# Kernel tuning notes

Hardware: AMD Instinct MI355X
Metric: run time of the kernel (lower is better)

The kernel has to match this reference:

```python
import jax, jax.numpy as jnp
import numpy as np

WS = 16      # window_size
FW = 1       # focal_window -> 3x3 grid of focal windows
FF = 2       # focal_factor (avg-pool for non-center windows)
NH = 8       # num_heads

_OFFSETS = [(di, dj) for di in range(-FW, FW + 1) for dj in range(-FW, FW + 1)]
# tokens contributed by each focal window (center keeps full res, neighbors pooled)
_COUNTS = np.array([WS * WS if (di == 0 and dj == 0) else (WS // FF) ** 2 for di, dj in _OFFSETS])
# center window gets zero bias, peripheral windows get -position_bias (intent of add_focal_bias)
_MULTS = np.array([0.0 if (di == 0 and dj == 0) else -1.0 for di, dj in _OFFSETS], dtype=np.float32)


def _gather_focal(x):
    """x: (B,H,W,C) -> (B*nW, kv_len, C) focal key/value tokens per window."""
    B, H, W, C = x.shape
    nH, nWg = H // WS, W // WS
    xp = jnp.pad(x, ((0, 0), (WS, WS), (WS, WS), (0, 0)), mode='reflect')
    # padded window grid: (B, nH+2, nWg+2, WS, WS, C)
    g = xp.reshape(B, nH + 2, WS, nWg + 2, WS, C).transpose(0, 1, 3, 2, 4, 5)
    parts = []
    for di, dj in _OFFSETS:
        w = g[:, 1 + di:1 + di + nH, 1 + dj:1 + dj + nWg]  # (B,nH,nWg,WS,WS,C)
        if di == 0 and dj == 0:
            t = w.reshape(B, nH, nWg, WS * WS, C)
        else:
            p = WS // FF  # avg_pool2d(kernel=stride=FF)
            t = w.reshape(B, nH, nWg, p, FF, p, FF, C).mean(axis=(4, 6)).reshape(B, nH, nWg, p * p, C)
        parts.append(t)
    kv = jnp.concatenate(parts, axis=3)  # (B,nH,nWg,kv_len,C)
    return kv.reshape(B * nH * nWg, -1, C)


def _bias_tokens(position_bias):
    # (NH, 9) -> (NH, kv_len): per-focal-window bias broadcast over its tokens
    scaled = position_bias * jnp.asarray(_MULTS)[None, :]
    return jnp.repeat(scaled, _COUNTS, axis=1)


def reference(x, Wq, bq, Wk, bk, Wv, bv, Wo, bo, position_bias):
    B, H, W, C = x.shape
    hd = C // NH
    scale = hd ** -0.5
    nH, nWg = H // WS, W // WS
    # window partition: (B*nW, WS*WS, C)
    xw = x.reshape(B, nH, WS, nWg, WS, C).transpose(0, 1, 3, 2, 4, 5).reshape(-1, WS * WS, C)
    kv = _gather_focal(x)  # (B*nW, kv_len, C)
    q = (xw @ Wq + bq).reshape(-1, WS * WS, NH, hd).transpose(0, 2, 1, 3)
    k = (kv @ Wk + bk).reshape(kv.shape[0], -1, NH, hd).transpose(0, 2, 1, 3)
    v = (kv @ Wv + bv).reshape(kv.shape[0], -1, NH, hd).transpose(0, 2, 1, 3)
    attn = jnp.einsum('whqd,whkd->whqk', q, k) * scale
    attn = attn + _bias_tokens(position_bias)[None, :, None, :]
    attn = jax.nn.softmax(attn, axis=-1)
    out = jnp.einsum('whqk,whkd->whqd', attn, v).transpose(0, 2, 1, 3).reshape(-1, WS * WS, C)
    out = out @ Wo + bo
    # window reverse
    out = out.reshape(B, nH, nWg, WS, WS, C).transpose(0, 1, 3, 2, 4, 5).reshape(B, H, W, C)
    return out


def setup_inputs() -> dict:
    key = jax.random.key(0)
    ks = jax.random.split(key, 10)
    D = 384
    w = lambda k: jax.random.normal(k, (D, D), dtype=jnp.float32) * 0.02
    b = lambda k: jax.random.normal(k, (D,), dtype=jnp.float32) * 0.02
    return {
        'x': jax.random.normal(ks[0], (2, 128, 128, D), dtype=jnp.float32),
        'Wq': w(ks[1]), 'bq': b(ks[2]),
        'Wk': w(ks[3]), 'bk': b(ks[4]),
        'Wv': w(ks[5]), 'bv': b(ks[6]),
        'Wo': w(ks[7]), 'bo': b(ks[8]),
        'position_bias': jax.random.normal(ks[9], (NH, 9), dtype=jnp.float32) * 0.02,
    }
```

## Files before the change

### kernel.cpp

```cpp
#include <hip/hip_runtime.h>
#include <hip/hip_bf16.h>

#define NTOK 32768
#define LOG2E 1.4426950408889634f

typedef __attribute__((ext_vector_type(8))) short bf16x8;
typedef __attribute__((ext_vector_type(4))) float f32x4;

__device__ __forceinline__ float bf2f(unsigned short u) {
  return __uint_as_float(((unsigned int)u) << 16);
}
__device__ __forceinline__ unsigned short f2bf(float f) {
  union { __hip_bfloat16 h; unsigned short u; } cv;
  cv.h = __float2bfloat16(f);
  return cv.u;
}
__device__ __forceinline__ unsigned cvt_pk_bf16(float lo, float hi) {
  unsigned r;
  asm("v_cvt_pk_bf16_f32 %0, %1, %2" : "=v"(r) : "v"(lo), "v"(hi));
  return r;
}
__device__ __forceinline__ float fast_exp2(float x) {
#if __has_builtin(__builtin_amdgcn_exp2f)
  return __builtin_amdgcn_exp2f(x);
#else
  return exp2f(x);
#endif
}

__device__ __forceinline__ void gload16(const void* g, void* l) {
  __builtin_amdgcn_global_load_lds(
      (const __attribute__((address_space(1))) unsigned int*)(unsigned long long)g,
      (__attribute__((address_space(3))) unsigned int*)(unsigned long long)l, 16, 0, 0);
}

__global__ __launch_bounds__(256) void convert_x(const float* __restrict__ x,
                                                 unsigned short* __restrict__ xb) {
  const int i = (blockIdx.x * 256 + threadIdx.x) * 8;
  float4 a = *(const float4*)(x + i);
  float4 b = *(const float4*)(x + i + 4);
  *(ushort4*)(xb + i)     = make_ushort4(f2bf(a.x), f2bf(a.y), f2bf(a.z), f2bf(a.w));
  *(ushort4*)(xb + i + 4) = make_ushort4(f2bf(b.x), f2bf(b.y), f2bf(b.z), f2bf(b.w));
}

__global__ __launch_bounds__(256) void transpose_w(const float* __restrict__ Wq,
                                                   const float* __restrict__ Wk,
                                                   const float* __restrict__ Wv,
                                                   const float* __restrict__ Wo,
                                                   unsigned short* __restrict__ Wt) {
  __shared__ float tile[32][33];
  const int wsel = blockIdx.z;
  const float* W = (wsel == 0) ? Wq : (wsel == 1) ? Wk : (wsel == 2) ? Wv : Wo;
  unsigned short* out = Wt + (size_t)wsel * 147456;
  const int k0 = blockIdx.x * 32, n0 = blockIdx.y * 32;
  const int r = threadIdx.x >> 3, c4 = (threadIdx.x & 7) * 4;
  float4 v = *(const float4*)&W[(size_t)(k0 + r) * 384 + n0 + c4];
  tile[r][c4 + 0] = v.x; tile[r][c4 + 1] = v.y; tile[r][c4 + 2] = v.z; tile[r][c4 + 3] = v.w;
  __syncthreads();
  ushort4 o = make_ushort4(f2bf(tile[c4 + 0][r]), f2bf(tile[c4 + 1][r]),
                           f2bf(tile[c4 + 2][r]), f2bf(tile[c4 + 3][r]));
  *(ushort4*)&out[(size_t)(n0 + r) * 384 + k0 + c4] = o;
}

__global__ __launch_bounds__(128) void pool_kernel(const unsigned short* __restrict__ xb,
                                                   unsigned short* __restrict__ P) {
  int blk = blockIdx.x;
  int b = blk / 6400;
  int rem = blk - b * 6400;
  int p0 = rem / 80, p1 = rem - p0 * 80;
  int i0 = 2 * p0 - 16, i1 = i0 + 1;
  int j0 = 2 * p1 - 16, j1 = j0 + 1;
  int r0 = i0 < 0 ? -i0 : (i0 > 127 ? 254 - i0 : i0);
  int r1 = i1 < 0 ? -i1 : (i1 > 127 ? 254 - i1 : i1);
  int c0 = j0 < 0 ? -j0 : (j0 > 127 ? 254 - j0 : j0);
  int c1 = j1 < 0 ? -j1 : (j1 > 127 ? 254 - j1 : j1);
  const unsigned short* s00 = xb + (((size_t)b * 128 + r0) * 128 + c0) * 384;
  const unsigned short* s01 = xb + (((size_t)b * 128 + r0) * 128 + c1) * 384;
  const unsigned short* s10 = xb + (((size_t)b * 128 + r1) * 128 + c0) * 384;
  const unsigned short* s11 = xb + (((size_t)b * 128 + r1) * 128 + c1) * 384;
  unsigned short* dst = P + (size_t)blk * 384;
  for (int c = threadIdx.x; c < 384; c += 128)
    dst[c] = f2bf(0.25f * (bf2f(s00[c]) + bf2f(s01[c]) + bf2f(s10[c]) + bf2f(s11[c])));
}

__global__ __launch_bounds__(256) void mfma_proj_fused(
    const unsigned short* __restrict__ xb, const unsigned short* __restrict__ P,
    const unsigned short* __restrict__ Wt,
    const float* __restrict__ bq, const float* __restrict__ bk, const float* __restrict__ bv,
    unsigned short* __restrict__ Qb, unsigned short* __restrict__ Kcat,
    unsigned short* __restrict__ Vcat) {
  const int bid = blockIdx.x;
  const unsigned short* X;
  int wsel, colblk, yy; size_t off;
  if (bid < 2304) {
    const int xx = bid % 9; yy = bid / 9;
    X = xb; wsel = xx / 3; colblk = xx % 3; off = 0;
  } else {
    const int r = bid - 2304; const int xx = r % 6; yy = r / 6;
    X = P; wsel = 1 + xx / 3; colblk = xx % 3; off = (size_t)NTOK * 384;
  }
  const float* bias = (wsel == 0) ? bq : (wsel == 1) ? bk : bv;
  unsigned short* Y = ((wsel == 0) ? Qb : (wsel == 1) ? Kcat : Vcat) + off;
  const unsigned short* Wm = Wt + (size_t)wsel * 147456;
  const int n0 = colblk * 128;
  const int m0 = yy * 128;

  __shared__ __attribute__((aligned(16))) unsigned short As[128 * 32];
  __shared__ __attribute__((aligned(16))) unsigned short Bs[128 * 32];
  const int t = threadIdx.x;
  const int w = t >> 6, l = t & 63, l15 = l & 15, g = l >> 4;
  const int wm = w >> 1, wn = w & 1;

  f32x4 acc[4][4];
  #pragma unroll
  for (int i = 0; i < 4; ++i)
    #pragma unroll
    for (int j = 0; j < 4; ++j) acc[i][j] = {0.f, 0.f, 0.f, 0.f};

  for (int k0 = 0; k0 < 384; k0 += 32) {
    __syncthreads();
    #pragma unroll
    for (int a = 0; a < 2; ++a) {
      const int c = w * 2 + a;
      const int row = c * 16 + (l >> 2), kc = (l & 3) * 8;
      gload16(X  + (size_t)(m0 + row) * 384 + k0 + kc, As + c * 512);
      gload16(Wm + (size_t)(n0 + row) * 384 + k0 + kc, Bs + c * 512);
    }
    __syncthreads();
    bf16x8 af[4], bfr[4];
    #pragma unroll
    for (int mi = 0; mi < 4; ++mi)
      af[mi] = *(const bf16x8*)(As + (wm * 64 + mi * 16 + l15) * 32 + g * 8);
    #pragma unroll
    for (int nj = 0; nj < 4; ++nj)
      bfr[nj] = *(const bf16x8*)(Bs + (wn * 64 + nj * 16 + l15) * 32 + g * 8);
    #pragma unroll
    for (int mi = 0; mi < 4; ++mi)
      #pragma unroll
      for (int nj = 0; nj < 4; ++nj)
        acc[mi][nj] = __builtin_amdgcn_mfma_f32_16x16x32_bf16(af[mi], bfr[nj], acc[mi][nj], 0, 0, 0);
  }

  float bv4[4];
  #pragma unroll
  for (int nj = 0; nj < 4; ++nj) bv4[nj] = bias[n0 + wn * 64 + nj * 16 + l15];
  #pragma unroll
  for (int mi = 0; mi < 4; ++mi)
    #pragma unroll
    for (int nj = 0; nj < 4; ++nj)
      #pragma unroll
      for (int r = 0; r < 4; ++r) {
        const size_t row = m0 + wm * 64 + mi * 16 + g * 4 + r;
        const size_t col = n0 + wn * 64 + nj * 16 + l15;
        Y[row * 384 + col] = f2bf(acc[mi][nj][r] + bv4[nj]);
      }
}

__global__ __launch_bounds__(256) void mfma_proj_out(const unsigned short* __restrict__ X,
                                                     const unsigned short* __restrict__ Wm,
                                                     const float* __restrict__ bias,
                                                     float* __restrict__ Y) {
  const int n0 = blockIdx.x * 128, m0 = blockIdx.y * 128;
  __shared__ __attribute__((aligned(16))) unsigned short As[128 * 32];
  __shared__ __attribute__((aligned(16))) unsigned short Bs[128 * 32];
  const int t = threadIdx.x;
  const int w = t >> 6, l = t & 63, l15 = l & 15, g = l >> 4;
  const int wm = w >> 1, wn = w & 1;

  f32x4 acc[4][4];
  #pragma unroll
  for (int i = 0; i < 4; ++i)
    #pragma unroll
    for (int j = 0; j < 4; ++j) acc[i][j] = {0.f, 0.f, 0.f, 0.f};

  for (int k0 = 0; k0 < 384; k0 += 32) {
    __syncthreads();
    #pragma unroll
    for (int a = 0; a < 2; ++a) {
      const int c = w * 2 + a;
      const int row = c * 16 + (l >> 2), kc = (l & 3) * 8;
      gload16(X  + (size_t)(m0 + row) * 384 + k0 + kc, As + c * 512);
      gload16(Wm + (size_t)(n0 + row) * 384 + k0 + kc, Bs + c * 512);
    }
    __syncthreads();
    bf16x8 af[4], bfr[4];
    #pragma unroll
    for (int mi = 0; mi < 4; ++mi)
      af[mi] = *(const bf16x8*)(As + (wm * 64 + mi * 16 + l15) * 32 + g * 8);
    #pragma unroll
    for (int nj = 0; nj < 4; ++nj)
      bfr[nj] = *(const bf16x8*)(Bs + (wn * 64 + nj * 16 + l15) * 32 + g * 8);
    #pragma unroll
    for (int mi = 0; mi < 4; ++mi)
      #pragma unroll
      for (int nj = 0; nj < 4; ++nj)
        acc[mi][nj] = __builtin_amdgcn_mfma_f32_16x16x32_bf16(af[mi], bfr[nj], acc[mi][nj], 0, 0, 0);
  }

  float bv4[4];
  #pragma unroll
  for (int nj = 0; nj < 4; ++nj) bv4[nj] = bias[n0 + wn * 64 + nj * 16 + l15];
  #pragma unroll
  for (int mi = 0; mi < 4; ++mi)
    #pragma unroll
    for (int nj = 0; nj < 4; ++nj)
      #pragma unroll
      for (int r = 0; r < 4; ++r) {
        const size_t row = m0 + wm * 64 + mi * 16 + g * 4 + r;
        const size_t col = n0 + wn * 64 + nj * 16 + l15;
        Y[row * 384 + col] = acc[mi][nj][r] + bv4[nj];
      }
}

__global__ __launch_bounds__(256) void attn_mfma(const unsigned short* __restrict__ Qg,
                                                 const unsigned short* __restrict__ Kc,
                                                 const unsigned short* __restrict__ Vc,
                                                 const float* __restrict__ pb,
                                                 unsigned short* __restrict__ AttO) {
  __shared__ unsigned short kvb[768];
  __shared__ float tb2s[12];
  __shared__ __attribute__((aligned(16))) unsigned short Ks[2][3072];
  __shared__ __attribute__((aligned(16))) unsigned short Vt[2][64 * 68];

  const int t = threadIdx.x;
  const int head = blockIdx.x >> 7, win = blockIdx.x & 127;
  const int b = win >> 6, wrem = win & 63, wi = wrem >> 3, wj = wrem & 7;
  const int w = t >> 6, l = t & 63, l15 = l & 15, g = l >> 4;
  const int hb = head * 48;

  for (int j = t; j < 768; j += 256) {
    int o, within;
    if (j < 256)      { o = j >> 6;               within = j & 63; }
    else if (j < 512) { o = 4;                    within = j - 256; }
    else              { o = 5 + ((j - 512) >> 6); within = j & 63; }
    int tok;
    if (o == 4) {
      int r = within >> 4, c = within & 15;
      tok = (b * 128 + wi * 16 + r) * 128 + wj * 16 + c;
    } else {
      int di = o / 3 - 1, dj = o - (o / 3) * 3 - 1;
      int t0 = within >> 3, t1 = within & 7;
      int p0 = 8 * (1 + di + wi) + t0, p1 = 8 * (1 + dj + wj) + t1;
      tok = NTOK + (b * 80 + p0) * 80 + p1;
    }
    kvb[j] = (unsigned short)tok;
  }
  if (t < 12) {
    int o = (t < 4) ? t : ((t < 8) ? 4 : t - 3);
    tb2s[t] = (o == 4) ? 0.0f : (-pb[head * 9 + o] * LOG2E);
  }
  for (int idx = t; idx < 2 * 16 * 68; idx += 256) {
    const int bu = idx / 1088, rem = idx - bu * 1088;
    const int rr = rem / 68, cc = rem - rr * 68;
    Vt[bu][(48 + rr) * 68 + cc] = (rr == 0) ? 0x3F80 : 0;
  }

  const float SCALE2 = 0.14433756729740643f * LOG2E;
  const bf16x8 z8 = {0, 0, 0, 0, 0, 0, 0, 0};

  bf16x8 qf[4][2];
  #pragma unroll
  for (int nf = 0; nf < 4; ++nf) {
    const int tok = ((b * 128 + wi * 16 + w * 4 + nf) * 128 + wj * 16 + l15);
    const unsigned short* qp = Qg + (size_t)tok * 384 + hb;
    qf[nf][0] = *(const bf16x8*)(qp + g * 8);
    qf[nf][1] = (g < 2) ? *(const bf16x8*)(qp + 32 + g * 8) : z8;
  }

  f32x4 Oacc[4][4];
  #pragma unroll
  for (int mo = 0; mo < 4; ++mo)
    #pragma unroll
    for (int nf = 0; nf < 4; ++nf) Oacc[mo][nf] = {0.f, 0.f, 0.f, 0.f};

  __syncthreads();

  uint4 va0, va1;
  {
    const int kvb0 = (int)kvb[l] * 384 + hb;
    gload16(Kc + kvb0 + w * 8, &Ks[0][w * 512]);
    if (w < 2) gload16(Kc + kvb0 + (4 + w) * 8, &Ks[0][(4 + w) * 512]);
    va0 = *(const uint4*)(Vc + kvb0 + w * 8);
    va1 = (w < 2) ? *(const uint4*)(Vc + kvb0 + (4 + w) * 8) : make_uint4(0, 0, 0, 0);
  }

  for (int T = 0; T < 12; ++T) {
    const int buf = T & 1;
    asm volatile("s_waitcnt vmcnt(0)" ::: "memory");
    {
      const unsigned short* u0 = (const unsigned short*)&va0;
      #pragma unroll
      for (int s = 0; s < 8; ++s) Vt[buf][(w * 8 + s) * 68 + l] = u0[s];
      if (w < 2) {
        const unsigned short* u1 = (const unsigned short*)&va1;
        #pragma unroll
        for (int s = 0; s < 8; ++s) Vt[buf][((4 + w) * 8 + s) * 68 + l] = u1[s];
      }
    }
    __syncthreads();
    if (T < 11) {
      const int kvb2 = (int)kvb[(T + 1) * 64 + l] * 384 + hb;
      gload16(Kc + kvb2 + w * 8, &Ks[buf ^ 1][w * 512]);
      if (w < 2) gload16(Kc + kvb2 + (4 + w) * 8, &Ks[buf ^ 1][(4 + w) * 512]);
      va0 = *(const uint4*)(Vc + kvb2 + w * 8);
      if (w < 2) va1 = *(const uint4*)(Vc + kvb2 + (4 + w) * 8);
    }

    const float tb = tb2s[T];
    #pragma unroll
    for (int h = 0; h < 2; ++h) {
      bf16x8 ka[2][2];
      #pragma unroll
      for (int mi = 0; mi < 2; ++mi) {
        const int krow = h * 32 + mi * 16 + l15;
        ka[mi][0] = *(const bf16x8*)&Ks[buf][g * 512 + krow * 8];
        ka[mi][1] = *(const bf16x8*)&Ks[buf][(4 + (g & 1)) * 512 + krow * 8];
      }
      f32x4 sf[2][4];
      #pragma unroll
      for (int mi = 0; mi < 2; ++mi)
        #pragma unroll
        for (int nf = 0; nf < 4; ++nf) sf[mi][nf] = {0.f, 0.f, 0.f, 0.f};
      __builtin_amdgcn_s_setprio(1);
      #pragma unroll
      for (int mi = 0; mi < 2; ++mi)
        #pragma unroll
        for (int nf = 0; nf < 4; ++nf) {
          sf[mi][nf] = __builtin_amdgcn_mfma_f32_16x16x32_bf16(ka[mi][0], qf[nf][0], sf[mi][nf], 0, 0, 0);
          sf[mi][nf] = __builtin_amdgcn_mfma_f32_16x16x32_bf16(ka[mi][1], qf[nf][1], sf[mi][nf], 0, 0, 0);
        }
      __builtin_amdgcn_s_setprio(0);

      bf16x8 pbf[4];
      #pragma unroll
      for (int nf = 0; nf < 4; ++nf) {
        float p[8];
        #pragma unroll
        for (int r = 0; r < 4; ++r) {
          p[r]     = fast_exp2(fmaf(sf[0][nf][r], SCALE2, tb));
          p[4 + r] = fast_exp2(fmaf(sf[1][nf][r], SCALE2, tb));
        }
        unsigned a0 = cvt_pk_bf16(p[0], p[1]);
        unsigned a1 = cvt_pk_bf16(p[2], p[3]);
        unsigned b0 = cvt_pk_bf16(p[4], p[5]);
        unsigned b1 = cvt_pk_bf16(p[6], p[7]);
        asm("v_permlane32_swap_b32 %0, %1" : "+v"(a0), "+v"(b0));
        asm("v_permlane32_swap_b32 %0, %1" : "+v"(a1), "+v"(b1));
        asm("v_permlane16_swap_b32 %0, %1" : "+v"(a0), "+v"(b0));
        asm("v_permlane16_swap_b32 %0, %1" : "+v"(a1), "+v"(b1));
        union { bf16x8 v; unsigned u[4]; } cv;
        cv.u[0] = a0; cv.u[1] = a1; cv.u[2] = b0; cv.u[3] = b1;
        pbf[nf] = cv.v;
      }

      #pragma unroll
      for (int mo = 0; mo < 4; ++mo) {
        const unsigned short* vp = &Vt[buf][(mo * 16 + l15) * 68 + h * 32 + g * 8];
        union { bf16x8 v; ushort4 u[2]; } cv;
        cv.u[0] = *(const ushort4*)vp;
        cv.u[1] = *(const ushort4*)(vp + 4);
        bf16x8 va = cv.v;
        __builtin_amdgcn_s_setprio(1);
        #pragma unroll
        for (int nf = 0; nf < 4; ++nf)
          Oacc[mo][nf] = __builtin_amdgcn_mfma_f32_16x16x32_bf16(va, pbf[nf], Oacc[mo][nf], 0, 0, 0);
        __builtin_amdgcn_s_setprio(0);
      }
    }
  }

  #pragma unroll
  for (int nf = 0; nf < 4; ++nf) {
    const float denom = __shfl(Oacc[3][nf][0], l15, 64);
    const float inv = 1.0f / denom;
    const int tok = ((b * 128 + wi * 16 + w * 4 + nf) * 128 + wj * 16 + l15);
    unsigned short* op = AttO + (size_t)tok * 384 + hb;
    #pragma unroll
    for (int mo = 0; mo < 3; ++mo) {
      uint2 u;
      u.x = cvt_pk_bf16(Oacc[mo][nf][0] * inv, Oacc[mo][nf][1] * inv);
      u.y = cvt_pk_bf16(Oacc[mo][nf][2] * inv, Oacc[mo][nf][3] * inv);
      *(uint2*)(op + mo * 16 + g * 4) = u;
    }
  }
}

extern "C" void kernel_launch(void* const* d_in, const int* in_sizes, int n_in,
                              void* d_out, int out_size, void* d_ws, size_t ws_size,
                              hipStream_t stream) {
  const float* x  = (const float*)d_in[0];
  const float* Wq = (const float*)d_in[1];
  const float* bq = (const float*)d_in[2];
  const float* Wk = (const float*)d_in[3];
  const float* bk = (const float*)d_in[4];
  const float* Wv = (const float*)d_in[5];
  const float* bv = (const float*)d_in[6];
  const float* Wo = (const float*)d_in[7];
  const float* bo = (const float*)d_in[8];
  const float* pb = (const float*)d_in[9];

  char* ws = (char*)d_ws;
  unsigned short* Wt   = (unsigned short*)(ws);
  unsigned short* P    = (unsigned short*)(ws + 1179648ull);
  unsigned short* Kcat = (unsigned short*)(ws + 11010048ull);
  unsigned short* Vcat = (unsigned short*)(ws + 46006272ull);
  unsigned short* xb   = (unsigned short*)(ws + 81002496ull);
  unsigned short* AttO = xb;
  unsigned short* Qb   = (unsigned short*)d_out;

  convert_x<<<6144, 256, 0, stream>>>(x, xb);
  pool_kernel<<<12800, 128, 0, stream>>>(xb, P);
  transpose_w<<<dim3(12, 12, 4), 256, 0, stream>>>(Wq, Wk, Wv, Wo, Wt);
  mfma_proj_fused<<<2904, 256, 0, stream>>>(xb, P, Wt, bq, bk, bv, Qb, Kcat, Vcat);
  attn_mfma<<<1024, 256, 0, stream>>>(Qb, Kcat, Vcat, pb, AttO);
  mfma_proj_out<<<dim3(3, 256), 256, 0, stream>>>(AttO, Wt + 3 * 147456, bo, (float*)d_out);
}
```

Baseline: 193.0 us.

## Double-buffer LDS in projection GEMMs and vectorize pool kernel

Both projection GEMM kernels now use two LDS buffers, so the global-to-LDS loads for the next K tile are issued before the MFMAs on the current tile, with one barrier per iteration instead of two. The pool kernel is remapped so each thread handles eight channels using 16-byte vector loads and stores, with fewer, larger blocks. This doubles LDS use per GEMM block, which may lower occupancy, in exchange for hiding global load latency behind compute.

After: 189.1 us. 2.1% less time.

```diff
diff --git a/kernel.cpp b/kernel.cpp
--- a/kernel.cpp
+++ b/kernel.cpp
@@ -62,25 +62,37 @@
   *(ushort4*)&out[(size_t)(n0 + r) * 384 + k0 + c4] = o;
 }
 
-__global__ __launch_bounds__(128) void pool_kernel(const unsigned short* __restrict__ xb,
+__global__ __launch_bounds__(192) void pool_kernel(const unsigned short* __restrict__ xb,
                                                    unsigned short* __restrict__ P) {
-  int blk = blockIdx.x;
-  int b = blk / 6400;
-  int rem = blk - b * 6400;
-  int p0 = rem / 80, p1 = rem - p0 * 80;
-  int i0 = 2 * p0 - 16, i1 = i0 + 1;
-  int j0 = 2 * p1 - 16, j1 = j0 + 1;
-  int r0 = i0 < 0 ? -i0 : (i0 > 127 ? 254 - i0 : i0);
-  int r1 = i1 < 0 ? -i1 : (i1 > 127 ? 254 - i1 : i1);
-  int c0 = j0 < 0 ? -j0 : (j0 > 127 ? 254 - j0 : j0);
-  int c1 = j1 < 0 ? -j1 : (j1 > 127 ? 254 - j1 : j1);
-  const unsigned short* s00 = xb + (((size_t)b * 128 + r0) * 128 + c0) * 384;
-  const unsigned short* s01 = xb + (((size_t)b * 128 + r0) * 128 + c1) * 384;
-  const unsigned short* s10 = xb + (((size_t)b * 128 + r1) * 128 + c0) * 384;
-  const unsigned short* s11 = xb + (((size_t)b * 128 + r1) * 128 + c1) * 384;
-  unsigned short* dst = P + (size_t)blk * 384;
-  for (int c = threadIdx.x; c < 384; c += 128)
-    dst[c] = f2bf(0.25f * (bf2f(s00[c]) + bf2f(s01[c]) + bf2f(s10[c]) + bf2f(s11[c])));
+  const int unit = blockIdx.x * 192 + threadIdx.x;
+  const int cell = unit / 48;
+  const int c8 = (unit - cell * 48) * 8;
+  const int b = cell / 6400;
+  const int rem = cell - b * 6400;
+  const int p0 = rem / 80, p1 = rem - p0 * 80;
+  const int i0 = 2 * p0 - 16, i1 = i0 + 1;
+  const int j0 = 2 * p1 - 16, j1 = j0 + 1;
+  const int r0 = i0 < 0 ? -i0 : (i0 > 127 ? 254 - i0 : i0);
+  const int r1 = i1 < 0 ? -i1 : (i1 > 127 ? 254 - i1 : i1);
+  const int c0 = j0 < 0 ? -j0 : (j0 > 127 ? 254 - j0 : j0);
+  const int c1 = j1 < 0 ? -j1 : (j1 > 127 ? 254 - j1 : j1);
+  uint4 u00 = *(const uint4*)(xb + ((size_t)((b * 128 + r0) * 128 + c0)) * 384 + c8);
+  uint4 u01 = *(const uint4*)(xb + ((size_t)((b * 128 + r0) * 128 + c1)) * 384 + c8);
+  uint4 u10 = *(const uint4*)(xb + ((size_t)((b * 128 + r1) * 128 + c0)) * 384 + c8);
+  uint4 u11 = *(const uint4*)(xb + ((size_t)((b * 128 + r1) * 128 + c1)) * 384 + c8);
+  const unsigned short* a0 = (const unsigned short*)&u00;
+  const unsigned short* a1 = (const unsigned short*)&u01;
+  const unsigned short* a2 = (const unsigned short*)&u10;
+  const unsigned short* a3 = (const unsigned short*)&u11;
+  unsigned short o[8];
+  #pragma unroll
+  for (int j = 0; j < 8; ++j)
+    o[j] = f2bf(0.25f * (bf2f(a0[j]) + bf2f(a1[j]) + bf2f(a2[j]) + bf2f(a3[j])));
+  uint4 ov;
+  unsigned short* op = (unsigned short*)&ov;
+  #pragma unroll
+  for (int j = 0; j < 8; ++j) op[j] = o[j];
+  *(uint4*)(P + (size_t)cell * 384 + c8) = ov;
 }
 
 __global__ __launch_bounds__(256) void mfma_proj_fused(
@@ -105,11 +117,13 @@
   const int n0 = colblk * 128;
   const int m0 = yy * 128;
 
-  __shared__ __attribute__((aligned(16))) unsigned short As[128 * 32];
-  __shared__ __attribute__((aligned(16))) unsigned short Bs[128 * 32];
+  __shared__ __attribute__((aligned(16))) unsigned short As[2][128 * 32];
+  __shared__ __attribute__((aligned(16))) unsigned short Bs[2][128 * 32];
   const int t = threadIdx.x;
   const int w = t >> 6, l = t & 63, l15 = l & 15, g = l >> 4;
   const int wm = w >> 1, wn = w & 1;
+  const int srow = (w * 2) * 16 + (l >> 2), srow2 = (w * 2 + 1) * 16 + (l >> 2);
+  const int skc = (l & 3) * 8;
 
   f32x4 acc[4][4];
   #pragma unroll
@@ -117,28 +131,43 @@
     #pragma unroll
     for (int j = 0; j < 4; ++j) acc[i][j] = {0.f, 0.f, 0.f, 0.f};
 
-  for (int k0 = 0; k0 < 384; k0 += 32) {
-    __syncthreads();
-    #pragma unroll
-    for (int a = 0; a < 2; ++a) {
-      const int c = w * 2 + a;
-      const int row = c * 16 + (l >> 2), kc = (l & 3) * 8;
-      gload16(X  + (size_t)(m0 + row) * 384 + k0 + kc, As + c * 512);
-      gload16(Wm + (size_t)(n0 + row) * 384 + k0 + kc, Bs + c * 512);
-    }
-    __syncthreads();
+  {
+    gload16(X  + (size_t)(m0 + srow)  * 384 + skc, &As[0][(w * 2)     * 512]);
+    gload16(X  + (size_t)(m0 + srow2) * 384 + skc, &As[0][(w * 2 + 1) * 512]);
+    gload16(Wm + (size_t)(n0 + srow)  * 384 + skc, &Bs[0][(w * 2)     * 512]);
+    gload16(Wm + (size_t)(n0 + srow2) * 384 + skc, &Bs[0][(w * 2 + 1) * 512]);
+  }
+  asm volatile("s_waitcnt vmcnt(0)" ::: "memory");
+  __builtin_amdgcn_s_barrier();
+  __builtin_amdgcn_sched_barrier(0);
+
+  int cur = 0;
+  for (int kt = 0; kt < 12; ++kt) {
+    if (kt < 11) {
+      const int k0 = (kt + 1) * 32;
+      gload16(X  + (size_t)(m0 + srow)  * 384 + k0 + skc, &As[cur ^ 1][(w * 2)     * 512]);
+      gload16(X  + (size_t)(m0 + srow2) * 384 + k0 + skc, &As[cur ^ 1][(w * 2 + 1) * 512]);
+      gload16(Wm + (size_t)(n0 + srow)  * 384 + k0 + skc, &Bs[cur ^ 1][(w * 2)     * 512]);
+      gload16(Wm + (size_t)(n0 + srow2) * 384 + k0 + skc, &Bs[cur ^ 1][(w * 2 + 1) * 512]);
+    }
     bf16x8 af[4], bfr[4];
     #pragma unroll
     for (int mi = 0; mi < 4; ++mi)
-      af[mi] = *(const bf16x8*)(As + (wm * 64 + mi * 16 + l15) * 32 + g * 8);
+      af[mi] = *(const bf16x8*)(&As[cur][(wm * 64 + mi * 16 + l15) * 32 + g * 8]);
     #pragma unroll
     for (int nj = 0; nj < 4; ++nj)
-      bfr[nj] = *(const bf16x8*)(Bs + (wn * 64 + nj * 16 + l15) * 32 + g * 8);
+      bfr[nj] = *(const bf16x8*)(&Bs[cur][(wn * 64 + nj * 16 + l15) * 32 + g * 8]);
     #pragma unroll
     for (int mi = 0; mi < 4; ++mi)
       #pragma unroll
       for (int nj = 0; nj < 4; ++nj)
         acc[mi][nj] = __builtin_amdgcn_mfma_f32_16x16x32_bf16(af[mi], bfr[nj], acc[mi][nj], 0, 0, 0);
+    if (kt < 11) {
+      asm volatile("s_waitcnt vmcnt(0)" ::: "memory");
+      __builtin_amdgcn_s_barrier();
+      __builtin_amdgcn_sched_barrier(0);
+      cur ^= 1;
+    }
   }
 
   float bv4[4];
@@ -161,11 +190,13 @@
                                                      const float* __restrict__ bias,
                                                      float* __restrict__ Y) {
   const int n0 = blockIdx.x * 128, m0 = blockIdx.y * 128;
-  __shared__ __attribute__((aligned(16))) unsigned short As[128 * 32];
-  __shared__ __attribute__((aligned(16))) unsigned short Bs[128 * 32];
+  __shared__ __attribute__((aligned(16))) unsigned short As[2][128 * 32];
+  __shared__ __attribute__((aligned(16))) unsigned short Bs[2][128 * 32];
   const int t = threadIdx.x;
   const int w = t >> 6, l = t & 63, l15 = l & 15, g = l >> 4;
   const int wm = w >> 1, wn = w & 1;
+  const int srow = (w * 2) * 16 + (l >> 2), srow2 = (w * 2 + 1) * 16 + (l >> 2);
+  const int skc = (l & 3) * 8;
 
   f32x4 acc[4][4];
   #pragma unroll
@@ -173,28 +204,43 @@
     #pragma unroll
     for (int j = 0; j < 4; ++j) acc[i][j] = {0.f, 0.f, 0.f, 0.f};
 
-  for (int k0 = 0; k0 < 384; k0 += 32) {
-    __syncthreads();
-    #pragma unroll
-    for (int a = 0; a < 2; ++a) {
-      const int c = w * 2 + a;
-      const int row = c * 16 + (l >> 2), kc = (l & 3) * 8;
-      gload16(X  + (size_t)(m0 + row) * 384 + k0 + kc, As + c * 512);
-      gload16(Wm + (size_t)(n0 + row) * 384 + k0 + kc, Bs + c * 512);
-    }
-    __syncthreads();
+  {
+    gload16(X  + (size_t)(m0 + srow)  * 384 + skc, &As[0][(w * 2)     * 512]);
+    gload16(X  + (size_t)(m0 + srow2) * 384 + skc, &As[0][(w * 2 + 1) * 512]);
+    gload16(Wm + (size_t)(n0 + srow)  * 384 + skc, &Bs[0][(w * 2)     * 512]);
+    gload16(Wm + (size_t)(n0 + srow2) * 384 + skc, &Bs[0][(w * 2 + 1) * 512]);
+  }
+  asm volatile("s_waitcnt vmcnt(0)" ::: "memory");
+  __builtin_amdgcn_s_barrier();
+  __builtin_amdgcn_sched_barrier(0);
+
+  int cur = 0;
+  for (int kt = 0; kt < 12; ++kt) {
+    if (kt < 11) {
+      const int k0 = (kt + 1) * 32;
+      gload16(X  + (size_t)(m0 + srow)  * 384 + k0 + skc, &As[cur ^ 1][(w * 2)     * 512]);
+      gload16(X  + (size_t)(m0 + srow2) * 384 + k0 + skc, &As[cur ^ 1][(w * 2 + 1) * 512]);
+      gload16(Wm + (size_t)(n0 + srow)  * 384 + k0 + skc, &Bs[cur ^ 1][(w * 2)     * 512]);
+      gload16(Wm + (size_t)(n0 + srow2) * 384 + k0 + skc, &Bs[cur ^ 1][(w * 2 + 1) * 512]);
+    }
     bf16x8 af[4], bfr[4];
     #pragma unroll
     for (int mi = 0; mi < 4; ++mi)
-      af[mi] = *(const bf16x8*)(As + (wm * 64 + mi * 16 + l15) * 32 + g * 8);
+      af[mi] = *(const bf16x8*)(&As[cur][(wm * 64 + mi * 16 + l15) * 32 + g * 8]);
     #pragma unroll
     for (int nj = 0; nj < 4; ++nj)
-      bfr[nj] = *(const bf16x8*)(Bs + (wn * 64 + nj * 16 + l15) * 32 + g * 8);
+      bfr[nj] = *(const bf16x8*)(&Bs[cur][(wn * 64 + nj * 16 + l15) * 32 + g * 8]);
     #pragma unroll
     for (int mi = 0; mi < 4; ++mi)
       #pragma unroll
       for (int nj = 0; nj < 4; ++nj)
         acc[mi][nj] = __builtin_amdgcn_mfma_f32_16x16x32_bf16(af[mi], bfr[nj], acc[mi][nj], 0, 0, 0);
+    if (kt < 11) {
+      asm volatile("s_waitcnt vmcnt(0)" ::: "memory");
+      __builtin_amdgcn_s_barrier();
+      __builtin_amdgcn_sched_barrier(0);
+      cur ^= 1;
+    }
   }
 
   float bv4[4];
@@ -409,7 +455,7 @@
   unsigned short* Qb   = (unsigned short*)d_out;
 
   convert_x<<<6144, 256, 0, stream>>>(x, xb);
-  pool_kernel<<<12800, 128, 0, stream>>>(xb, P);
+  pool_kernel<<<3200, 192, 0, stream>>>(xb, P);
   transpose_w<<<dim3(12, 12, 4), 256, 0, stream>>>(Wq, Wk, Wv, Wo, Wt);
   mfma_proj_fused<<<2904, 256, 0, stream>>>(xb, P, Wt, bq, bk, bv, Qb, Kcat, Vcat);
   attn_mfma<<<1024, 256, 0, stream>>>(Qb, Kcat, Vcat, pb, AttO);
```
